# Optimization experiments

Hardware: AMD Instinct MI355X
Metric: run time of the kernel (lower is better)

## Reference

```python
import jax, jax.numpy as jnp
import numpy as np

F_NODES = 16384   # number of function nodes
DEG = 8           # in-degree == out-degree per function node
E = F_NODES * DEG # edge-latent dimension (num edges)
B = 64            # batch
H = 16            # hidden_channels of each per-node MLP
LAYERS = 10       # GSNN layers (weights shared across layers)


def setup_inputs() -> dict:
    key = jax.random.key(0)
    k0, k1, k2, k3 = jax.random.split(key, 4)
    x0 = jax.random.normal(k0, (B, E), dtype=jnp.float32)
    # each edge has exactly one destination function node -> in_ixs is a permutation of edges
    in_ixs = jax.random.permutation(k1, E).reshape(F_NODES, DEG)
    # per-node 2-layer MLP weights: in_degree -> H -> out_degree
    W1 = jax.random.normal(k2, (F_NODES, H, DEG), dtype=jnp.float32) * (1.0 / np.sqrt(DEG))
    b1 = jnp.zeros((F_NODES, H), dtype=jnp.float32)
    W2 = jax.random.normal(k3, (F_NODES, DEG, H), dtype=jnp.float32) * (1.0 / np.sqrt(H))
    b2 = jnp.zeros((F_NODES, DEG), dtype=jnp.float32)
    return {"x0": x0, "W1": W1, "b1": b1, "W2": W2, "b2": b2, "in_ixs": in_ixs}


def reference(x0, W1, b1, W2, b2, in_ixs):
    # x0: [B, E] edge-latent input. Each layer: every function node gathers its
    # in-edges, applies its own small MLP, scatters to its out-edges; results are
    # summed into x_new and a residual x0 is added (GSNN.forward).
    x = x0
    for _ in range(LAYERS):
        g = x[:, in_ixs]                                   # [B, F, DEG] gather in-edge values
        h = jax.nn.elu(jnp.einsum('bfd,fhd->bfh', g, W1) + b1)  # [B, F, H]
        o = jnp.einsum('bfh,foh->bfo', h, W2) + b2         # [B, F, DEG]
        # out-edges of node f are the contiguous slots f*DEG:(f+1)*DEG (disjoint scatter)
        x = o.reshape(x0.shape) + x0                       # sum of node scatters + residual
    return x
```

## Files before the change

### kernel.cpp

```cpp
#include <hip/hip_runtime.h>
#include <math.h>

#define F_NODES 16384
#define DEG 8
#define E_TOT (F_NODES * DEG)
#define B 64
#define H 16
#define LAYERS 10
#define NPW 2

typedef unsigned short bf16_t;

__device__ __forceinline__ bf16_t f32_to_bf16(float f)
{
    unsigned u = __float_as_uint(f);
    u = (u + 0x7FFFu + ((u >> 16) & 1u)) >> 16;
    return (bf16_t)u;
}
__device__ __forceinline__ float bf16_to_f32(bf16_t h)
{
    return __uint_as_float((unsigned)h << 16);
}
__device__ __forceinline__ float bfu_lo(unsigned u) { return __uint_as_float(u << 16); }
__device__ __forceinline__ float bfu_hi(unsigned u) { return __uint_as_float(u & 0xFFFF0000u); }

__global__ __launch_bounds__(256) void transpose_in_kernel(
    const float* __restrict__ x0, bf16_t* __restrict__ xT16)
{
    __shared__ float tile[64 * 65];
    const int e0 = blockIdx.x * 64;
    const int c  = threadIdx.x & 63;
    const int r  = threadIdx.x >> 6;

    #pragma unroll
    for (int i = 0; i < 16; ++i) {
        const int b = r + i * 4;
        tile[c * 65 + b] = x0[(size_t)b * E_TOT + e0 + c];
    }
    __syncthreads();
    const int b = threadIdx.x & 63;
    #pragma unroll
    for (int i = 0; i < 16; ++i) {
        const int el = r + i * 4;
        xT16[(size_t)(e0 + el) * B + b] = f32_to_bf16(tile[el * 65 + b]);
    }
}

__global__ __launch_bounds__(256) void build_inv_kernel(
    const int* __restrict__ in_ixs, int* __restrict__ inv)
{
    const int k = blockIdx.x * 256 + threadIdx.x;
    inv[in_ixs[k]] = k;
}

__global__ __launch_bounds__(256) void pack_weights_kernel(
    const float* __restrict__ W1, const float* __restrict__ W2,
    unsigned* __restrict__ W1b, unsigned* __restrict__ W2b)
{
    const int i = blockIdx.x * 256 + threadIdx.x;
    float2 a = ((const float2*)W1)[i];
    W1b[i] = (unsigned)f32_to_bf16(a.x) | ((unsigned)f32_to_bf16(a.y) << 16);
    float2 c = ((const float2*)W2)[i];
    W2b[i] = (unsigned)f32_to_bf16(c.x) | ((unsigned)f32_to_bf16(c.y) << 16);
}

__device__ __forceinline__ float fast_elu(float x)
{
    float e = __builtin_amdgcn_exp2f(x * 1.44269504088896340736f) - 1.0f;
    return x > 0.0f ? x : e;
}

template <int MODE>
__global__ __launch_bounds__(256) void layer_kernel(
    const bf16_t*  __restrict__ zin,
    const bf16_t*  __restrict__ x0T16,
    const unsigned* __restrict__ W1b,
    const float*   __restrict__ b1,
    const unsigned* __restrict__ W2b,
    const float*   __restrict__ b2,
    const int*     __restrict__ in_ixs,
    const int*     __restrict__ inv,
    bf16_t* __restrict__ zout,
    float*  __restrict__ out)
{
    const int lane    = threadIdx.x & 63;
    const int wv      = threadIdx.x >> 6;
    const int wave_id = (int)blockIdx.x * 4 + wv;

    #pragma unroll
    for (int n = 0; n < NPW; ++n) {
        const int f = __builtin_amdgcn_readfirstlane(wave_id * NPW + n);

        float g[DEG], r[DEG];
        {
            const bf16_t* rp = x0T16 + (size_t)f * DEG * B + lane;
            if (MODE == 0) {
                const int* ixp = in_ixs + f * DEG;
                #pragma unroll
                for (int d = 0; d < DEG; ++d) {
                    g[d] = bf16_to_f32(x0T16[(size_t)ixp[d] * B + lane]);
                    r[d] = bf16_to_f32(rp[d * B]);
                }
            } else {
                const bf16_t* zp = zin + (size_t)f * DEG * B + lane;
                #pragma unroll
                for (int d = 0; d < DEG; ++d) {
                    g[d] = bf16_to_f32(zp[d * B]);
                    r[d] = bf16_to_f32(rp[d * B]);
                }
            }
        }

        const unsigned* w1 = W1b + f * (H * DEG / 2);
        const float*   bb1 = b1 + f * H;
        float h[H];
        #pragma unroll
        for (int j = 0; j < H; ++j) {
            float acc = bb1[j];
            #pragma unroll
            for (int dp = 0; dp < DEG / 2; ++dp) {
                const unsigned u = w1[j * (DEG / 2) + dp];
                acc = fmaf(bfu_lo(u), g[2 * dp],     acc);
                acc = fmaf(bfu_hi(u), g[2 * dp + 1], acc);
            }
            h[j] = fast_elu(acc);
        }

        const unsigned* w2 = W2b + f * (DEG * H / 2);
        const float*   bb2 = b2 + f * DEG;
        float o[DEG];
        #pragma unroll
        for (int d = 0; d < DEG; ++d) {
            float acc = bb2[d];
            #pragma unroll
            for (int jp = 0; jp < H / 2; ++jp) {
                const unsigned u = w2[d * (H / 2) + jp];
                acc = fmaf(bfu_lo(u), h[2 * jp],     acc);
                acc = fmaf(bfu_hi(u), h[2 * jp + 1], acc);
            }
            o[d] = acc + r[d];
        }

        if (MODE == 2) {
            float4 v0 = make_float4(o[0], o[1], o[2], o[3]);
            float4 v1 = make_float4(o[4], o[5], o[6], o[7]);
            float4* dst = (float4*)(out + (size_t)lane * E_TOT + f * DEG);
            dst[0] = v0;
            dst[1] = v1;
        } else {
            const int* invp = inv + f * DEG;
            #pragma unroll
            for (int d = 0; d < DEG; ++d)
                zout[(size_t)invp[d] * B + lane] = f32_to_bf16(o[d]);
        }
    }
}

extern "C" void kernel_launch(void* const* d_in, const int* in_sizes, int n_in,
                              void* d_out, int out_size, void* d_ws, size_t ws_size,
                              hipStream_t stream)
{
    const float* x0     = (const float*)d_in[0];
    const float* W1     = (const float*)d_in[1];
    const float* b1     = (const float*)d_in[2];
    const float* W2     = (const float*)d_in[3];
    const float* b2     = (const float*)d_in[4];
    const int*   in_ixs = (const int*)d_in[5];
    float* out = (float*)d_out;

    const size_t NEL = (size_t)E_TOT * B;
    bf16_t*   x0T16 = (bf16_t*)d_ws;
    bf16_t*   zA    = x0T16 + NEL;
    bf16_t*   zB    = zA + NEL;
    int*      inv   = (int*)(zB + NEL);
    unsigned* W1b   = (unsigned*)(inv + E_TOT);
    unsigned* W2b   = W1b + F_NODES * H * DEG / 2;

    transpose_in_kernel<<<E_TOT / 64, 256, 0, stream>>>(x0, x0T16);
    build_inv_kernel<<<E_TOT / 256, 256, 0, stream>>>(in_ixs, inv);
    pack_weights_kernel<<<F_NODES * H * DEG / 2 / 256, 256, 0, stream>>>(
        W1, W2, W1b, W2b);

    const int grid = F_NODES / (4 * NPW);

    layer_kernel<0><<<grid, 256, 0, stream>>>(
        nullptr, x0T16, W1b, b1, W2b, b2, in_ixs, inv, zA, nullptr);

    const bf16_t* cur = zA;
    bf16_t* nxt = zB;
    for (int l = 1; l < LAYERS - 1; ++l) {
        layer_kernel<1><<<grid, 256, 0, stream>>>(
            cur, x0T16, W1b, b1, W2b, b2, in_ixs, inv, nxt, nullptr);
        cur = nxt;
        nxt = (nxt == zA) ? zB : zA;
    }

    layer_kernel<2><<<grid, 256, 0, stream>>>(
        cur, x0T16, W1b, b1, W2b, b2, in_ixs, inv, nullptr, out);
}
```

Measured before the change: 295.0 us.

## Gather via LDS-staged 16-byte loads and write contiguous outputs instead of inverse scatter

Each layer now stages its block's 16 nodes in shared memory. Gathered in-edge rows and residual rows are loaded as 128-byte edge rows using uint4 loads. Outputs are written back to LDS and then stored contiguously, which removes the inverse-permutation scatter and the build_inv kernel; the gather now happens on the read side through in_ixs. The block grows to 16 nodes, using 32 KB of LDS and an extra barrier, which may lower occupancy.

```diff
diff --git a/kernel.cpp b/kernel.cpp
--- a/kernel.cpp
+++ b/kernel.cpp
@@ -7,7 +7,10 @@
 #define B 64
 #define H 16
 #define LAYERS 10
-#define NPW 2
+
+#define NPB 16
+#define TPB 256
+#define GRIDN (F_NODES / NPB)
 
 typedef unsigned short bf16_t;
 
@@ -44,13 +47,6 @@
         const int el = r + i * 4;
         xT16[(size_t)(e0 + el) * B + b] = f32_to_bf16(tile[el * 65 + b]);
     }
-}
-
-__global__ __launch_bounds__(256) void build_inv_kernel(
-    const int* __restrict__ in_ixs, int* __restrict__ inv)
-{
-    const int k = blockIdx.x * 256 + threadIdx.x;
-    inv[in_ixs[k]] = k;
 }
 
 __global__ __launch_bounds__(256) void pack_weights_kernel(
@@ -70,45 +66,52 @@
     return x > 0.0f ? x : e;
 }
 
-template <int MODE>
-__global__ __launch_bounds__(256) void layer_kernel(
-    const bf16_t*  __restrict__ zin,
-    const bf16_t*  __restrict__ x0T16,
+template <bool FINAL>
+__global__ __launch_bounds__(TPB) void layer_kernel(
+    const bf16_t*   __restrict__ zsrc,
+    const bf16_t*   __restrict__ x0T16,
     const unsigned* __restrict__ W1b,
-    const float*   __restrict__ b1,
+    const float*    __restrict__ b1,
     const unsigned* __restrict__ W2b,
-    const float*   __restrict__ b2,
-    const int*     __restrict__ in_ixs,
-    const int*     __restrict__ inv,
+    const float*    __restrict__ b2,
+    const int*      __restrict__ in_ixs,
     bf16_t* __restrict__ zout,
     float*  __restrict__ out)
 {
-    const int lane    = threadIdx.x & 63;
-    const int wv      = threadIdx.x >> 6;
-    const int wave_id = (int)blockIdx.x * 4 + wv;
-
-    #pragma unroll
-    for (int n = 0; n < NPW; ++n) {
-        const int f = __builtin_amdgcn_readfirstlane(wave_id * NPW + n);
+    __shared__ uint4 ldsG4[NPB * 8 * 8];
+    __shared__ uint4 ldsR4[NPB * 8 * 8];
+
+    const int t   = threadIdx.x;
+    const int f0  = (int)blockIdx.x * NPB;
+    const size_t e0 = (size_t)f0 * DEG;
+
+    const uint4* resp = (const uint4*)(x0T16 + e0 * B);
+    #pragma unroll
+    for (int rnd = 0; rnd < 4; ++rnd) {
+        const int slot = rnd * TPB + t;
+        const int j = slot >> 3;
+        const int p = slot & 7;
+        const int k = in_ixs[e0 + j];
+        ldsG4[slot] = ((const uint4*)(zsrc + (size_t)k * B))[p];
+        ldsR4[slot] = resp[slot];
+    }
+    __syncthreads();
+
+    const int lane = t & 63;
+    const int wv   = t >> 6;
+    const unsigned short* ldsG = (const unsigned short*)ldsG4;
+    const unsigned short* ldsR = (const unsigned short*)ldsR4;
+
+    #pragma unroll
+    for (int n = 0; n < 4; ++n) {
+        const int q = wv * 4 + n;
+        const int f = __builtin_amdgcn_readfirstlane(f0 + q);
 
         float g[DEG], r[DEG];
-        {
-            const bf16_t* rp = x0T16 + (size_t)f * DEG * B + lane;
-            if (MODE == 0) {
-                const int* ixp = in_ixs + f * DEG;
-                #pragma unroll
-                for (int d = 0; d < DEG; ++d) {
-                    g[d] = bf16_to_f32(x0T16[(size_t)ixp[d] * B + lane]);
-                    r[d] = bf16_to_f32(rp[d * B]);
-                }
-            } else {
-                const bf16_t* zp = zin + (size_t)f * DEG * B + lane;
-                #pragma unroll
-                for (int d = 0; d < DEG; ++d) {
-                    g[d] = bf16_to_f32(zp[d * B]);
-                    r[d] = bf16_to_f32(rp[d * B]);
-                }
-            }
+        #pragma unroll
+        for (int d = 0; d < DEG; ++d) {
+            g[d] = bf16_to_f32(ldsG[(q * DEG + d) * B + lane]);
+            r[d] = bf16_to_f32(ldsR[(q * DEG + d) * B + lane]);
         }
 
         const unsigned* w1 = W1b + f * (H * DEG / 2);
@@ -141,17 +144,27 @@
             o[d] = acc + r[d];
         }
 
-        if (MODE == 2) {
+        if (FINAL) {
             float4 v0 = make_float4(o[0], o[1], o[2], o[3]);
             float4 v1 = make_float4(o[4], o[5], o[6], o[7]);
             float4* dst = (float4*)(out + (size_t)lane * E_TOT + f * DEG);
             dst[0] = v0;
             dst[1] = v1;
         } else {
-            const int* invp = inv + f * DEG;
+            unsigned short* ldsW = (unsigned short*)ldsG4;
             #pragma unroll
             for (int d = 0; d < DEG; ++d)
-                zout[(size_t)invp[d] * B + lane] = f32_to_bf16(o[d]);
+                ldsW[(q * DEG + d) * B + lane] = f32_to_bf16(o[d]);
+        }
+    }
+
+    if (!FINAL) {
+        __syncthreads();
+        uint4* dst = (uint4*)(zout + e0 * B);
+        #pragma unroll
+        for (int rnd = 0; rnd < 4; ++rnd) {
+            const int slot = rnd * TPB + t;
+            dst[slot] = ldsG4[slot];
         }
     }
 }
@@ -172,29 +185,25 @@
     bf16_t*   x0T16 = (bf16_t*)d_ws;
     bf16_t*   zA    = x0T16 + NEL;
     bf16_t*   zB    = zA + NEL;
-    int*      inv   = (int*)(zB + NEL);
-    unsigned* W1b   = (unsigned*)(inv + E_TOT);
+    unsigned* W1b   = (unsigned*)(zB + NEL);
     unsigned* W2b   = W1b + F_NODES * H * DEG / 2;
 
     transpose_in_kernel<<<E_TOT / 64, 256, 0, stream>>>(x0, x0T16);
-    build_inv_kernel<<<E_TOT / 256, 256, 0, stream>>>(in_ixs, inv);
     pack_weights_kernel<<<F_NODES * H * DEG / 2 / 256, 256, 0, stream>>>(
         W1, W2, W1b, W2b);
 
-    const int grid = F_NODES / (4 * NPW);
-
-    layer_kernel<0><<<grid, 256, 0, stream>>>(
-        nullptr, x0T16, W1b, b1, W2b, b2, in_ixs, inv, zA, nullptr);
+    layer_kernel<false><<<GRIDN, TPB, 0, stream>>>(
+        x0T16, x0T16, W1b, b1, W2b, b2, in_ixs, zA, nullptr);
 
     const bf16_t* cur = zA;
     bf16_t* nxt = zB;
     for (int l = 1; l < LAYERS - 1; ++l) {
-        layer_kernel<1><<<grid, 256, 0, stream>>>(
-            cur, x0T16, W1b, b1, W2b, b2, in_ixs, inv, nxt, nullptr);
+        layer_kernel<false><<<GRIDN, TPB, 0, stream>>>(
+            cur, x0T16, W1b, b1, W2b, b2, in_ixs, nxt, nullptr);
         cur = nxt;
         nxt = (nxt == zA) ? zB : zA;
     }
 
-    layer_kernel<2><<<grid, 256, 0, stream>>>(
-        cur, x0T16, W1b, b1, W2b, b2, in_ixs, inv, nullptr, out);
-}
+    layer_kernel<true><<<GRIDN, TPB, 0, stream>>>(
+        cur, x0T16, W1b, b1, W2b, b2, in_ixs, nullptr, out);
+}
```

After: 351.8 us. 19.3% more time.
